# Optimization experiments

Hardware: AMD Instinct MI355X
Metric: run time of the kernel (lower is better)

Reference implementation:

```python
import jax, jax.numpy as jnp
import numpy as np

N_NODES = 100000
N_EDGES = 3200000


def gcn_conv(x, W, b, src, dst, n_nodes):
    """PyG GCNConv: self-loops, symmetric D^-1/2 A D^-1/2 norm, linear, bias."""
    loop = jnp.arange(n_nodes, dtype=src.dtype)
    s = jnp.concatenate([src, loop])  # [E+N]
    d = jnp.concatenate([dst, loop])  # [E+N]
    # degree computed at destination (col), edge_weight = 1
    deg = jax.ops.segment_sum(jnp.ones_like(d, dtype=x.dtype), d,
                              num_segments=n_nodes)
    dinv = jnp.where(deg > 0, jax.lax.rsqrt(deg), 0.0)
    norm = dinv[s] * dinv[d]  # [E+N]
    h = x @ W.T  # [N, out]
    msg = h[s] * norm[:, None]  # gather + scale, [E+N, out]
    out = jax.ops.segment_sum(msg, d, num_segments=n_nodes)  # scatter-add
    return out + b


def setup_inputs() -> dict:
    key = jax.random.key(0)
    k1, k2, k3, k4 = jax.random.split(key, 4)
    x = jax.random.normal(k1, (N_NODES, 2), dtype=jnp.float32)
    edge_index = jax.random.randint(k2, (2, N_EDGES), 0, N_NODES,
                                    dtype=jnp.int64)
    # Glorot-ish init for linear weights
    W1 = jax.random.normal(k3, (64, 2), dtype=jnp.float32) * 0.5
    b1 = jnp.zeros((64,), dtype=jnp.float32)
    W2 = jax.random.normal(k4, (2, 64), dtype=jnp.float32) * 0.125
    b2 = jnp.zeros((2,), dtype=jnp.float32)
    return {"x": x, "edge_index": edge_index, "W1": W1, "b1": b1,
            "W2": W2, "b2": b2}


def reference(x, edge_index, W1, b1, W2, b2):
    src, dst = edge_index[0], edge_index[1]
    h = gcn_conv(x, W1, b1, src, dst, N_NODES)
    h = jax.nn.relu(h)
    out = gcn_conv(h, W2, b2, src, dst, N_NODES)
    return out
```

## Files before the change

### kernel.cpp

```cpp
#include <hip/hip_runtime.h>

#define N_NODES 100000
#define SHIFT 9
#define BNODES 512
#define NB 196
#define CAP 18432
#define TILE 8192
#define SB 512


__global__ __launch_bounds__(SB) void k_sort(const int* __restrict__ src,
                                             const int* __restrict__ dst,
                                             int* claim, int* sg, int e) {
    __shared__ int hist[NB];
    __shared__ int scanb[256];
    __shared__ int start[NB];
    __shared__ int runbase[NB];
    __shared__ int stage[TILE];
    __shared__ unsigned char binmap[TILE];

    const int t = threadIdx.x;
    const int base = blockIdx.x * TILE;
    const int n = min(TILE, e - base);

    for (int i = t; i < NB; i += SB) hist[i] = 0;
    __syncthreads();

    int recs[16];
    int bins[16];
#pragma unroll
    for (int k = 0; k < 4; ++k) {
        int idx = base + (k * SB + t) * 4;
        if (idx + 3 < e) {
            int4 s4 = *(const int4*)(src + idx);
            int4 d4 = *(const int4*)(dst + idx);
            int ss[4] = {s4.x, s4.y, s4.z, s4.w};
            int dd[4] = {d4.x, d4.y, d4.z, d4.w};
#pragma unroll
            for (int j = 0; j < 4; ++j) {
                int b = dd[j] >> SHIFT;
                bins[4 * k + j] = b;
                recs[4 * k + j] = ss[j] | ((dd[j] & (BNODES - 1)) << 17);
                atomicAdd(&hist[b], 1);
            }
        } else {
#pragma unroll
            for (int j = 0; j < 4; ++j) {
                int i2 = idx + j;
                if (i2 < e) {
                    int d = dst[i2];
                    int b = d >> SHIFT;
                    bins[4 * k + j] = b;
                    recs[4 * k + j] = src[i2] | ((d & (BNODES - 1)) << 17);
                    atomicAdd(&hist[b], 1);
                } else {
                    bins[4 * k + j] = -1;
                }
            }
        }
    }
    __syncthreads();

    if (t < 256) scanb[t] = (t < NB) ? hist[t] : 0;
    __syncthreads();
    for (int off = 1; off < 256; off <<= 1) {
        int w = (t < 256 && t >= off) ? scanb[t - off] : 0;
        __syncthreads();
        if (t < 256) scanb[t] += w;
        __syncthreads();
    }
    if (t < NB) {
        int c = hist[t];
        int excl = scanb[t] - c;
        start[t] = excl;
        scanb[t] = excl;
        runbase[t] = c ? atomicAdd(&claim[t], c) : 0;
    }
    __syncthreads();

#pragma unroll
    for (int m = 0; m < 16; ++m) {
        int b = bins[m];
        if (b >= 0) {
            int pos = atomicAdd(&scanb[b], 1);
            stage[pos] = recs[m];
            binmap[pos] = (unsigned char)b;
        }
    }
    __syncthreads();

    for (int i = t; i < n; i += SB) {
        int b = binmap[i];
        sg[b * CAP + runbase[b] + (i - start[b])] = stage[i];
    }
}

__global__ __launch_bounds__(1024) void k_refine(const int* __restrict__ claim,
                                                 const int* __restrict__ sg,
                                                 const float* __restrict__ x,
                                                 int* sg2, int* packed,
                                                 float2* u) {
    __shared__ int hist[BNODES];
    __shared__ int scanb[BNODES];
    const int t = threadIdx.x;
    const int b = blockIdx.x;
    const int* p = sg + b * CAP;
    const int len = claim[b];

    int4 r[5];
#pragma unroll
    for (int k = 0; k < 5; ++k) {
        int idx = 4 * t + 4096 * k;
        int4 v = make_int4(-1, -1, -1, -1);
        if (idx + 3 < len) v = *(const int4*)(p + idx);
        else if (idx < len) {
            v.x = p[idx];
            if (idx + 1 < len) v.y = p[idx + 1];
            if (idx + 2 < len) v.z = p[idx + 2];
        }
        r[k] = v;
    }
    if (t < BNODES) hist[t] = 0;
    __syncthreads();
#pragma unroll
    for (int k = 0; k < 5; ++k) {
        if (r[k].x != -1) atomicAdd(&hist[((unsigned)r[k].x) >> 17], 1);
        if (r[k].y != -1) atomicAdd(&hist[((unsigned)r[k].y) >> 17], 1);
        if (r[k].z != -1) atomicAdd(&hist[((unsigned)r[k].z) >> 17], 1);
        if (r[k].w != -1) atomicAdd(&hist[((unsigned)r[k].w) >> 17], 1);
    }
    __syncthreads();

    if (t < BNODES) scanb[t] = hist[t];
    __syncthreads();
    for (int off = 1; off < BNODES; off <<= 1) {
        int w = (t >= off && t < BNODES) ? scanb[t - off] : 0;
        __syncthreads();
        if (t < BNODES) scanb[t] += w;
        __syncthreads();
    }
    if (t < BNODES) {
        int mycnt = hist[t];
        int myexcl = scanb[t] - mycnt;
        int node = b * BNODES + t;
        if (node < N_NODES) {
            packed[node] = (b * CAP + myexcl) | (mycnt << 22);
            float dv = rsqrtf((float)(mycnt + 1));
            float2 xv = ((const float2*)x)[node];
            u[node] = make_float2(dv * xv.x, dv * xv.y);
        }
        hist[t] = myexcl;
    }
    __syncthreads();

    int* q = sg2 + b * CAP;
#pragma unroll
    for (int k = 0; k < 5; ++k) {
        if (r[k].x != -1) q[atomicAdd(&hist[((unsigned)r[k].x) >> 17], 1)] = r[k].x & 0x1FFFF;
        if (r[k].y != -1) q[atomicAdd(&hist[((unsigned)r[k].y) >> 17], 1)] = r[k].y & 0x1FFFF;
        if (r[k].z != -1) q[atomicAdd(&hist[((unsigned)r[k].z) >> 17], 1)] = r[k].z & 0x1FFFF;
        if (r[k].w != -1) q[atomicAdd(&hist[((unsigned)r[k].w) >> 17], 1)] = r[k].w & 0x1FFFF;
    }
}

__global__ __launch_bounds__(256) void k_agg1(const int* __restrict__ sg2,
                                              const int* __restrict__ packed,
                                              const float2* __restrict__ u,
                                              const float* __restrict__ W1,
                                              const float* __restrict__ b1,
                                              const float* __restrict__ W2,
                                              float2* v) {
    __shared__ float sW1[128], sb1[64], sW2[128];
    int t = threadIdx.x;
    if (t < 128) { sW1[t] = W1[t]; sW2[t] = W2[t]; }
    else if (t < 192) sb1[t - 128] = b1[t - 128];
    __syncthreads();
    int n = blockIdx.x * 256 + t;
    if (n >= N_NODES) return;
    int pk = packed[n];
    int s = pk & 0x3FFFFF;
    int cnt = ((unsigned)pk) >> 22;
    int e2 = s + cnt;
    float sx = 0.f, sy = 0.f;
    int i = s;
    for (; i + 8 <= e2; i += 8) {
        float2 g0 = u[sg2[i]],     g1 = u[sg2[i + 1]];
        float2 g2 = u[sg2[i + 2]], g3 = u[sg2[i + 3]];
        float2 g4 = u[sg2[i + 4]], g5 = u[sg2[i + 5]];
        float2 g6 = u[sg2[i + 6]], g7 = u[sg2[i + 7]];
        sx += ((g0.x + g1.x) + (g2.x + g3.x)) + ((g4.x + g5.x) + (g6.x + g7.x));
        sy += ((g0.y + g1.y) + (g2.y + g3.y)) + ((g4.y + g5.y) + (g6.y + g7.y));
    }
    for (; i < e2; ++i) { float2 g = u[sg2[i]]; sx += g.x; sy += g.y; }
    float dv = rsqrtf((float)(cnt + 1));
    float2 un = u[n];
    float a0 = dv * (sx + un.x), a1 = dv * (sy + un.y);
    float y0 = 0.f, y1 = 0.f;
#pragma unroll
    for (int j = 0; j < 64; ++j) {
        float h = fmaxf(fmaf(sW1[2 * j], a0,
                        fmaf(sW1[2 * j + 1], a1, sb1[j])), 0.f);
        y0 = fmaf(sW2[j], h, y0);
        y1 = fmaf(sW2[64 + j], h, y1);
    }
    v[n] = make_float2(dv * y0, dv * y1);
}

__global__ __launch_bounds__(256) void k_agg2(const int* __restrict__ sg2,
                                              const int* __restrict__ packed,
                                              const float2* __restrict__ v,
                                              const float* __restrict__ b2,
                                              float2* out) {
    int n = blockIdx.x * 256 + threadIdx.x;
    if (n >= N_NODES) return;
    int pk = packed[n];
    int s = pk & 0x3FFFFF;
    int cnt = ((unsigned)pk) >> 22;
    int e2 = s + cnt;
    float sx = 0.f, sy = 0.f;
    int i = s;
    for (; i + 8 <= e2; i += 8) {
        float2 g0 = v[sg2[i]],     g1 = v[sg2[i + 1]];
        float2 g2 = v[sg2[i + 2]], g3 = v[sg2[i + 3]];
        float2 g4 = v[sg2[i + 4]], g5 = v[sg2[i + 5]];
        float2 g6 = v[sg2[i + 6]], g7 = v[sg2[i + 7]];
        sx += ((g0.x + g1.x) + (g2.x + g3.x)) + ((g4.x + g5.x) + (g6.x + g7.x));
        sy += ((g0.y + g1.y) + (g2.y + g3.y)) + ((g4.y + g5.y) + (g6.y + g7.y));
    }
    for (; i < e2; ++i) { float2 g = v[sg2[i]]; sx += g.x; sy += g.y; }
    float dv = rsqrtf((float)(cnt + 1));
    float2 vn = v[n];
    out[n] = make_float2(fmaf(dv, sx + vn.x, b2[0]),
                         fmaf(dv, sy + vn.y, b2[1]));
}

extern "C" void kernel_launch(void* const* d_in, const int* in_sizes, int n_in,
                              void* d_out, int out_size, void* d_ws, size_t ws_size,
                              hipStream_t stream) {
    const float* x  = (const float*)d_in[0];
    const int* ei   = (const int*)d_in[1];
    const float* W1 = (const float*)d_in[2];
    const float* b1 = (const float*)d_in[3];
    const float* W2 = (const float*)d_in[4];
    const float* b2 = (const float*)d_in[5];

    int e = in_sizes[1] / 2;
    const int* src = ei;
    const int* dst = ei + e;

    int* ws      = (int*)d_ws;
    int* claim   = ws;
    int* sg      = ws + NB;
    int* sg2     = sg + NB * CAP;
    int* packed  = sg2 + NB * CAP;
    float2* u    = (float2*)(packed + N_NODES);
    float2* v    = u + N_NODES;
    float2* outp = (float2*)d_out;

    hipMemsetAsync(claim, 0, NB * sizeof(int), stream);

    const int gN = (N_NODES + 255) / 256;
    k_sort  <<<(e + TILE - 1) / TILE, SB, 0, stream>>>(src, dst, claim, sg, e);
    k_refine<<<NB, 1024, 0, stream>>>(claim, sg, x, sg2, packed, u);
    k_agg1  <<<gN, 256, 0, stream>>>(sg2, packed, u, W1, b1, W2, v);
    k_agg2  <<<gN, 256, 0, stream>>>(sg2, packed, v, b2, outp);
}
```

Baseline: 159.3 us.

## Use 8 threads per node in aggregation kernels with shuffle reductions

Both aggregation kernels change from one thread per node to eight threads per node. Each lane gathers a strided slice of the node's CSR neighbour list, and partial sums are combined with xor shuffles. The 64-wide MLP in agg1 is also split across the eight lanes. This coalesces the index reads and spreads out the per-node work imbalance (average degree about 32), at the cost of extra shuffles, redundant per-lane loads of packed/u, and eight times as many blocks.

New measurement: 153.7 us. 1.04x faster.

```diff
diff --git a/kernel.cpp b/kernel.cpp
--- a/kernel.cpp
+++ b/kernel.cpp
@@ -175,35 +175,41 @@
     if (t < 128) { sW1[t] = W1[t]; sW2[t] = W2[t]; }
     else if (t < 192) sb1[t - 128] = b1[t - 128];
     __syncthreads();
-    int n = blockIdx.x * 256 + t;
+    int n = blockIdx.x * 32 + (t >> 3);
     if (n >= N_NODES) return;
+    int g = t & 7;
     int pk = packed[n];
     int s = pk & 0x3FFFFF;
     int cnt = ((unsigned)pk) >> 22;
     int e2 = s + cnt;
     float sx = 0.f, sy = 0.f;
-    int i = s;
-    for (; i + 8 <= e2; i += 8) {
-        float2 g0 = u[sg2[i]],     g1 = u[sg2[i + 1]];
-        float2 g2 = u[sg2[i + 2]], g3 = u[sg2[i + 3]];
-        float2 g4 = u[sg2[i + 4]], g5 = u[sg2[i + 5]];
-        float2 g6 = u[sg2[i + 6]], g7 = u[sg2[i + 7]];
-        sx += ((g0.x + g1.x) + (g2.x + g3.x)) + ((g4.x + g5.x) + (g6.x + g7.x));
-        sy += ((g0.y + g1.y) + (g2.y + g3.y)) + ((g4.y + g5.y) + (g6.y + g7.y));
-    }
-    for (; i < e2; ++i) { float2 g = u[sg2[i]]; sx += g.x; sy += g.y; }
+    int i = s + g;
+    for (; i + 8 < e2; i += 16) {
+        float2 ga = u[sg2[i]];
+        float2 gb = u[sg2[i + 8]];
+        sx += ga.x + gb.x;
+        sy += ga.y + gb.y;
+    }
+    if (i < e2) { float2 ga = u[sg2[i]]; sx += ga.x; sy += ga.y; }
+    sx += __shfl_xor(sx, 1, 8); sy += __shfl_xor(sy, 1, 8);
+    sx += __shfl_xor(sx, 2, 8); sy += __shfl_xor(sy, 2, 8);
+    sx += __shfl_xor(sx, 4, 8); sy += __shfl_xor(sy, 4, 8);
     float dv = rsqrtf((float)(cnt + 1));
     float2 un = u[n];
     float a0 = dv * (sx + un.x), a1 = dv * (sy + un.y);
     float y0 = 0.f, y1 = 0.f;
 #pragma unroll
-    for (int j = 0; j < 64; ++j) {
+    for (int k = 0; k < 8; ++k) {
+        int j = g + 8 * k;
         float h = fmaxf(fmaf(sW1[2 * j], a0,
                         fmaf(sW1[2 * j + 1], a1, sb1[j])), 0.f);
         y0 = fmaf(sW2[j], h, y0);
         y1 = fmaf(sW2[64 + j], h, y1);
     }
-    v[n] = make_float2(dv * y0, dv * y1);
+    y0 += __shfl_xor(y0, 1, 8); y1 += __shfl_xor(y1, 1, 8);
+    y0 += __shfl_xor(y0, 2, 8); y1 += __shfl_xor(y1, 2, 8);
+    y0 += __shfl_xor(y0, 4, 8); y1 += __shfl_xor(y1, 4, 8);
+    if (g == 0) v[n] = make_float2(dv * y0, dv * y1);
 }
 
 __global__ __launch_bounds__(256) void k_agg2(const int* __restrict__ sg2,
@@ -211,27 +217,32 @@
                                               const float2* __restrict__ v,
                                               const float* __restrict__ b2,
                                               float2* out) {
-    int n = blockIdx.x * 256 + threadIdx.x;
+    int t = threadIdx.x;
+    int n = blockIdx.x * 32 + (t >> 3);
     if (n >= N_NODES) return;
+    int g = t & 7;
     int pk = packed[n];
     int s = pk & 0x3FFFFF;
     int cnt = ((unsigned)pk) >> 22;
     int e2 = s + cnt;
     float sx = 0.f, sy = 0.f;
-    int i = s;
-    for (; i + 8 <= e2; i += 8) {
-        float2 g0 = v[sg2[i]],     g1 = v[sg2[i + 1]];
-        float2 g2 = v[sg2[i + 2]], g3 = v[sg2[i + 3]];
-        float2 g4 = v[sg2[i + 4]], g5 = v[sg2[i + 5]];
-        float2 g6 = v[sg2[i + 6]], g7 = v[sg2[i + 7]];
-        sx += ((g0.x + g1.x) + (g2.x + g3.x)) + ((g4.x + g5.x) + (g6.x + g7.x));
-        sy += ((g0.y + g1.y) + (g2.y + g3.y)) + ((g4.y + g5.y) + (g6.y + g7.y));
-    }
-    for (; i < e2; ++i) { float2 g = v[sg2[i]]; sx += g.x; sy += g.y; }
-    float dv = rsqrtf((float)(cnt + 1));
-    float2 vn = v[n];
-    out[n] = make_float2(fmaf(dv, sx + vn.x, b2[0]),
-                         fmaf(dv, sy + vn.y, b2[1]));
+    int i = s + g;
+    for (; i + 8 < e2; i += 16) {
+        float2 ga = v[sg2[i]];
+        float2 gb = v[sg2[i + 8]];
+        sx += ga.x + gb.x;
+        sy += ga.y + gb.y;
+    }
+    if (i < e2) { float2 ga = v[sg2[i]]; sx += ga.x; sy += ga.y; }
+    sx += __shfl_xor(sx, 1, 8); sy += __shfl_xor(sy, 1, 8);
+    sx += __shfl_xor(sx, 2, 8); sy += __shfl_xor(sy, 2, 8);
+    sx += __shfl_xor(sx, 4, 8); sy += __shfl_xor(sy, 4, 8);
+    if (g == 0) {
+        float dv = rsqrtf((float)(cnt + 1));
+        float2 vn = v[n];
+        out[n] = make_float2(fmaf(dv, sx + vn.x, b2[0]),
+                             fmaf(dv, sy + vn.y, b2[1]));
+    }
 }
 
 extern "C" void kernel_launch(void* const* d_in, const int* in_sizes, int n_in,
@@ -259,9 +270,9 @@
 
     hipMemsetAsync(claim, 0, NB * sizeof(int), stream);
 
-    const int gN = (N_NODES + 255) / 256;
+    const int gA = (N_NODES + 31) / 32;
     k_sort  <<<(e + TILE - 1) / TILE, SB, 0, stream>>>(src, dst, claim, sg, e);
     k_refine<<<NB, 1024, 0, stream>>>(claim, sg, x, sg2, packed, u);
-    k_agg1  <<<gN, 256, 0, stream>>>(sg2, packed, u, W1, b1, W2, v);
-    k_agg2  <<<gN, 256, 0, stream>>>(sg2, packed, v, b2, outp);
-}
+    k_agg1  <<<gA, 256, 0, stream>>>(sg2, packed, u, W1, b1, W2, v);
+    k_agg2  <<<gA, 256, 0, stream>>>(sg2, packed, v, b2, outp);
+}
```
